# Kernel optimization log

Measured on AMD Instinct MI355X. Metric: run time of the kernel, lower is better.

The kernel has to match this reference:

```python
import math
import jax, jax.numpy as jnp
import numpy as np

B, S, HID = 1, 256, 1024
H, D = 16, 64
INV_NORM = 1.0 / math.sqrt(D)  # inv_norm_factor (beta = 1.0)
NEG = -1e9


def _bloom_alibi(num_heads, seq_len):
    # standard Bloom alibi slopes, shape [H, 1, S]
    closest_pow2 = 2 ** math.floor(math.log2(num_heads))
    base = 2.0 ** (-(2.0 ** -(math.log2(closest_pow2) - 3)))
    slopes = base ** np.arange(1, closest_pow2 + 1)
    if closest_pow2 != num_heads:
        extra_base = 2.0 ** (-(2.0 ** -(math.log2(2 * closest_pow2) - 3)))
        n_extra = min(closest_pow2, num_heads - closest_pow2)
        slopes = np.concatenate([slopes, extra_base ** np.arange(1, 1 + 2 * n_extra, 2)])
    pos = np.arange(seq_len, dtype=np.float32)[None, None, :]
    return jnp.asarray(slopes[:, None, None].astype(np.float32) * pos)  # [H,1,S]


def setup_inputs() -> dict:
    key = jax.random.key(0)
    ks = jax.random.split(key, 6)
    hidden_states = jax.random.normal(ks[0], (B, S, HID), jnp.float32)
    residual = jax.random.normal(ks[1], (B, S, HID), jnp.float32)
    alibi = _bloom_alibi(H, S)  # [B*H, 1, S] with B=1
    # additive causal mask [B, 1, S, S]
    causal = jnp.tril(jnp.ones((S, S), bool))
    attention_mask = jnp.where(causal, 0.0, NEG).astype(jnp.float32)[None, None]
    W_qkv = jax.random.normal(ks[2], (HID, 3 * HID), jnp.float32) * (1.0 / math.sqrt(HID))
    b_qkv = jax.random.normal(ks[3], (3 * HID,), jnp.float32) * 0.02
    W_dense = jax.random.normal(ks[4], (HID, HID), jnp.float32) * (1.0 / math.sqrt(HID))
    b_dense = jax.random.normal(ks[5], (HID,), jnp.float32) * 0.02
    return dict(hidden_states=hidden_states, residual=residual, alibi=alibi,
                attention_mask=attention_mask, W_qkv=W_qkv, b_qkv=b_qkv,
                W_dense=W_dense, b_dense=b_dense)


def reference(hidden_states, residual, alibi, attention_mask, W_qkv, b_qkv, W_dense, b_dense):
    b, s, _ = hidden_states.shape
    # fused qkv projection, Bloom layout: (B, S, H, 3, D)
    fused = (hidden_states @ W_qkv + b_qkv).reshape(b, s, H, 3, D)
    q = fused[..., 0, :].transpose(0, 2, 1, 3)  # [B,H,S,D]
    k = fused[..., 1, :].transpose(0, 2, 1, 3)
    v = fused[..., 2, :].transpose(0, 2, 1, 3)

    alibi_b = alibi.reshape(b, H, 1, s)  # broadcast over query dim
    # standard alibi attention scores: [B,H,S,S]
    scores = alibi_b + INV_NORM * jnp.einsum('bhid,bhjd->bhij', q, k)
    scores = scores + attention_mask  # mask applied only to full scores (as in source)
    # per-dim delta scores: [B,H,D,S,S]; delta[b,h,d,i,j] = alibi + inv_norm * q_d * k_d
    delta = alibi_b[:, :, None] + INV_NORM * jnp.einsum('bhid,bhjd->bhdij', q, k)

    diff = (scores[:, :, None] - delta) * (1.0 / math.sqrt(D))
    p_diff = jax.nn.softmax(diff.astype(jnp.float32), axis=-1)  # [B,H,D,S,S]
    p = jax.nn.softmax(scores.astype(jnp.float32), axis=-1)     # [B,H,S,S]

    # qk importance: sum over batch, query, key of squared deviation, per (h, d)
    qk_importance = jnp.sum((p_diff - p[:, :, None]) ** 2, axis=(0, 3, 4)).reshape(-1)  # [H*D]

    context = jnp.einsum('bhij,bhjd->bhid', p, v)  # [B,H,S,D]
    context = context.transpose(0, 2, 1, 3).reshape(b, s, H * D)
    out = context @ W_dense + b_dense
    out = out + residual  # eval mode: dropout is identity
    return out, qk_importance
```

## Files before the change

### kernel.cpp

```cpp
#include <hip/hip_runtime.h>
#include <math.h>

#define NH  16
#define SEQ 256
#define HD  64
#define HID 1024
#define N3  3072

#define OFF_QB   0
#define OFF_KB   131072
#define OFF_KTB  262144
#define OFF_VTB  393216
#define OFF_CTX  524288

typedef __attribute__((ext_vector_type(8))) short bf16x8;
typedef __attribute__((ext_vector_type(4))) float f32x4;
typedef __attribute__((ext_vector_type(2))) unsigned short us2;
typedef __attribute__((ext_vector_type(4))) unsigned short us4;
typedef __attribute__((ext_vector_type(8))) unsigned short us8;
typedef __attribute__((ext_vector_type(4))) unsigned u32x4;

__device__ __forceinline__ unsigned short f2bf(float x) {
  unsigned u = __builtin_bit_cast(unsigned, x);
  u += 0x7FFF + ((u >> 16) & 1);
  return (unsigned short)(u >> 16);
}
__device__ __forceinline__ float bf2f(unsigned short b) {
  return __builtin_bit_cast(float, (unsigned)b << 16);
}
__device__ __forceinline__ unsigned f2bf2(float lo, float hi) {
  unsigned r;
  asm("v_cvt_pk_bf16_f32 %0, %1, %2" : "=v"(r) : "v"(lo), "v"(hi));
  return r;
}

__global__ __launch_bounds__(256) void k_qkv(
    const float* __restrict__ A, const float* __restrict__ W,
    const float* __restrict__ bias, float* __restrict__ ws,
    float* __restrict__ out) {
  if (blockIdx.x == 0 && blockIdx.y < 4)
    out[SEQ * HID + blockIdx.y * 256 + threadIdx.x] = 0.f;
  __shared__ __align__(16) unsigned short As[32 * 72];
  __shared__ __align__(16) unsigned short Bs[32 * 72];
  const int tid = threadIdx.x;
  const int w = tid >> 6, lane = tid & 63;
  const int col = lane & 15, quad = lane >> 4;
  const int m0 = blockIdx.y * 32, n0 = blockIdx.x * 32;
  const int am = tid >> 3, ak = (tid & 7) * 8;
  const int bn = tid & 31, bkg = (tid >> 5) * 8;
  const float* Ap = &A[(m0 + am) * HID + ak];
  const float* Wp = W + n0 + bn;
  float4 a0 = *(const float4*)&Ap[0];
  float4 a1 = *(const float4*)&Ap[4];
  float pa[8];
#pragma unroll
  for (int u = 0; u < 8; ++u) pa[u] = Wp[(bkg + u) * N3];
  float4 c0 = *(const float4*)&Ap[64];
  float4 c1 = *(const float4*)&Ap[68];
  float pc[8];
#pragma unroll
  for (int u = 0; u < 8; ++u) pc[u] = Wp[(64 + bkg + u) * N3];
  f32x4 acc = {0.f, 0.f, 0.f, 0.f};
  const int k8 = quad * 8;
  const int mt = w & 1, nt = w >> 1;
  for (int k0 = 0; k0 < HID; k0 += 128) {
    *(u32x4*)&As[am * 72 + ak] =
        (u32x4){f2bf2(a0.x, a0.y), f2bf2(a0.z, a0.w),
                f2bf2(a1.x, a1.y), f2bf2(a1.z, a1.w)};
    *(u32x4*)&Bs[bn * 72 + bkg] =
        (u32x4){f2bf2(pa[0], pa[1]), f2bf2(pa[2], pa[3]),
                f2bf2(pa[4], pa[5]), f2bf2(pa[6], pa[7])};
    __syncthreads();
    const int ka = k0 + 128;
    if (ka < HID) {
      a0 = *(const float4*)&Ap[ka];
      a1 = *(const float4*)&Ap[ka + 4];
#pragma unroll
      for (int u = 0; u < 8; ++u) pa[u] = Wp[(ka + bkg + u) * N3];
    }
    {
      const bf16x8 af0 = *(const bf16x8*)&As[(mt * 16 + col) * 72 + k8];
      const bf16x8 af1 = *(const bf16x8*)&As[(mt * 16 + col) * 72 + k8 + 32];
      const bf16x8 bf0 = *(const bf16x8*)&Bs[(nt * 16 + col) * 72 + k8];
      const bf16x8 bf1 = *(const bf16x8*)&Bs[(nt * 16 + col) * 72 + k8 + 32];
      acc = __builtin_amdgcn_mfma_f32_16x16x32_bf16(af0, bf0, acc, 0, 0, 0);
      acc = __builtin_amdgcn_mfma_f32_16x16x32_bf16(af1, bf1, acc, 0, 0, 0);
    }
    __syncthreads();
    *(u32x4*)&As[am * 72 + ak] =
        (u32x4){f2bf2(c0.x, c0.y), f2bf2(c0.z, c0.w),
                f2bf2(c1.x, c1.y), f2bf2(c1.z, c1.w)};
    *(u32x4*)&Bs[bn * 72 + bkg] =
        (u32x4){f2bf2(pc[0], pc[1]), f2bf2(pc[2], pc[3]),
                f2bf2(pc[4], pc[5]), f2bf2(pc[6], pc[7])};
    __syncthreads();
    const int kb2 = k0 + 192;
    if (kb2 < HID) {
      c0 = *(const float4*)&Ap[kb2];
      c1 = *(const float4*)&Ap[kb2 + 4];
#pragma unroll
      for (int u = 0; u < 8; ++u) pc[u] = Wp[(kb2 + bkg + u) * N3];
    }
    {
      const bf16x8 af0 = *(const bf16x8*)&As[(mt * 16 + col) * 72 + k8];
      const bf16x8 af1 = *(const bf16x8*)&As[(mt * 16 + col) * 72 + k8 + 32];
      const bf16x8 bf0 = *(const bf16x8*)&Bs[(nt * 16 + col) * 72 + k8];
      const bf16x8 bf1 = *(const bf16x8*)&Bs[(nt * 16 + col) * 72 + k8 + 32];
      acc = __builtin_amdgcn_mfma_f32_16x16x32_bf16(af0, bf0, acc, 0, 0, 0);
      acc = __builtin_amdgcn_mfma_f32_16x16x32_bf16(af1, bf1, acc, 0, 0, 0);
    }
    __syncthreads();
  }
  unsigned short* qb  = (unsigned short*)(ws + OFF_QB);
  unsigned short* kb  = (unsigned short*)(ws + OFF_KB);
  unsigned short* ktb = (unsigned short*)(ws + OFF_KTB);
  unsigned short* vtb = (unsigned short*)(ws + OFF_VTB);
  const int n = n0 + nt * 16 + col;
  const int h = n / 192;
  const int r2 = n - h * 192;
  const int which = r2 >> 6, d = r2 & 63;
  const float bv = bias[n];
  const unsigned v01 = f2bf2(acc[0] + bv, acc[1] + bv);
  const unsigned v23 = f2bf2(acc[2] + bv, acc[3] + bv);
  const unsigned short vbr[4] = {
      (unsigned short)v01, (unsigned short)(v01 >> 16),
      (unsigned short)v23, (unsigned short)(v23 >> 16)};
#pragma unroll
  for (int r = 0; r < 4; ++r) {
    const int m = m0 + mt * 16 + quad * 4 + r;
    const unsigned short vb = vbr[r];
    if (which == 0) {
      qb[(h * SEQ + m) * HD + d] = vb;
    } else if (which == 1) {
      kb[(h * SEQ + m) * HD + d] = vb;
      ktb[(h * HD + d) * SEQ + m] = vb;
    } else {
      vtb[(h * HD + d) * SEQ + m] = vb;
    }
  }
}

__global__ __launch_bounds__(256) void k_attn(
    const float* __restrict__ alibi, float* __restrict__ ws,
    float* __restrict__ out) {
  *(float4*)&out[(blockIdx.x * 256 + threadIdx.x) * 4] =
      (float4){0.f, 0.f, 0.f, 0.f};
  const int bx = blockIdx.x;
  const int h = bx >> 4, i0 = (bx & 15) * 16;
  const int tid = threadIdx.x, w = tid >> 6, lane = tid & 63;
  const int col = lane & 15, quad = lane >> 4;
  __shared__ __align__(16) unsigned short Albs[3 * 16 * 280];
  __shared__ __align__(16) unsigned short plds[16 * 272];
  __shared__ __align__(16) float redm[16][4];
  __shared__ __align__(16) float reds[16][4];
  __shared__ __align__(16) float red4[16][4][4];
  __shared__ __align__(16) float rowsc[16][4];
  const unsigned short* qbh  = (const unsigned short*)(ws + OFF_QB) + h * SEQ * HD;
  const unsigned short* kbh  = (const unsigned short*)(ws + OFF_KB) + h * SEQ * HD;
  const unsigned short* ktbh = (const unsigned short*)(ws + OFF_KTB) + h * HD * SEQ;
  const unsigned short* vtbh = (const unsigned short*)(ws + OFF_VTB) + h * HD * SEQ;
  const bf16x8 a0 = *(const bf16x8*)&qbh[(i0 + col) * HD + quad * 8];
  const bf16x8 a1 = *(const bf16x8*)&qbh[(i0 + col) * HD + quad * 8 + 32];
  f32x4 acc[4] = {{0.f, 0.f, 0.f, 0.f}, {0.f, 0.f, 0.f, 0.f},
                  {0.f, 0.f, 0.f, 0.f}, {0.f, 0.f, 0.f, 0.f}};
#pragma unroll
  for (int t = 0; t < 4; ++t) {
    const int j = w * 64 + t * 16 + col;
    const bf16x8 b0 = *(const bf16x8*)&kbh[j * HD + quad * 8];
    const bf16x8 b1 = *(const bf16x8*)&kbh[j * HD + quad * 8 + 32];
    acc[t] = __builtin_amdgcn_mfma_f32_16x16x32_bf16(a0, b0, acc[t], 0, 0, 0);
    acc[t] = __builtin_amdgcn_mfma_f32_16x16x32_bf16(a1, b1, acc[t], 0, 0, 0);
  }
  float c[4][4], eb[4][4];
  float rmax[4] = {-3.0e38f, -3.0e38f, -3.0e38f, -3.0e38f};
#pragma unroll
  for (int t = 0; t < 4; ++t) {
    const int j = w * 64 + t * 16 + col;
    const float al = alibi[h * SEQ + j];
#pragma unroll
    for (int r = 0; r < 4; ++r) {
      const int i = i0 + quad * 4 + r;
      const float s = acc[t][r] * 0.125f;
      const float mv = (j <= i) ? 0.f : -1e9f;
      eb[t][r] = __expf((s + mv) * 0.125f);
      const float cv = al + s + mv;
      c[t][r] = cv;
      rmax[r] = fmaxf(rmax[r], cv);
    }
  }
#pragma unroll
  for (int r = 0; r < 4; ++r)
#pragma unroll
    for (int off = 1; off < 16; off <<= 1)
      rmax[r] = fmaxf(rmax[r], __shfl_xor(rmax[r], off));
  if (col == 0)
#pragma unroll
    for (int r = 0; r < 4; ++r) redm[quad * 4 + r][w] = rmax[r];
  __syncthreads();
  float rsum[4];
#pragma unroll
  for (int r = 0; r < 4; ++r) {
    const float4 m4 = *(const float4*)redm[quad * 4 + r];
    const float M = fmaxf(fmaxf(m4.x, m4.y), fmaxf(m4.z, m4.w));
    float s = 0.f;
#pragma unroll
    for (int t = 0; t < 4; ++t) {
      c[t][r] = __expf(c[t][r] - M);
      s += c[t][r];
    }
#pragma unroll
    for (int off = 1; off < 16; off <<= 1) s += __shfl_xor(s, off);
    rsum[r] = s;
  }
  if (col == 0)
#pragma unroll
    for (int r = 0; r < 4; ++r) reds[quad * 4 + r][w] = rsum[r];
  __syncthreads();
#pragma unroll
  for (int r = 0; r < 4; ++r) {
    const float4 s4 = *(const float4*)reds[quad * 4 + r];
    const float inv = __builtin_amdgcn_rcpf((s4.x + s4.y) + (s4.z + s4.w));
    const int il = quad * 4 + r;
    float pt[4];
    float s0 = 0.f, t0 = 0.f, u0 = 0.f, sp = 0.f;
#pragma unroll
    for (int t = 0; t < 4; ++t) {
      const float p = c[t][r] * inv;
      const float E = eb[t][r];
      pt[t] = p;
      s0 += E;
      t0 = __builtin_fmaf(E, E, t0);
      u0 = __builtin_fmaf(E, p, u0);
      sp = __builtin_fmaf(p, p, sp);
    }
    const int jb = il * 280 + w * 64 + col;
    const int pb = il * 272 + w * 64 + col;
    unsigned x;
    x = f2bf2(eb[0][r], eb[1][r]);
    Albs[jb] = (unsigned short)x; Albs[jb + 16] = (unsigned short)(x >> 16);
    x = f2bf2(eb[2][r], eb[3][r]);
    Albs[jb + 32] = (unsigned short)x; Albs[jb + 48] = (unsigned short)(x >> 16);
    x = f2bf2(eb[0][r] * eb[0][r], eb[1][r] * eb[1][r]);
    Albs[4480 + jb] = (unsigned short)x; Albs[4480 + jb + 16] = (unsigned short)(x >> 16);
    x = f2bf2(eb[2][r] * eb[2][r], eb[3][r] * eb[3][r]);
    Albs[4480 + jb + 32] = (unsigned short)x; Albs[4480 + jb + 48] = (unsigned short)(x >> 16);
    x = f2bf2(eb[0][r] * pt[0], eb[1][r] * pt[1]);
    Albs[8960 + jb] = (unsigned short)x; Albs[8960 + jb + 16] = (unsigned short)(x >> 16);
    x = f2bf2(eb[2][r] * pt[2], eb[3][r] * pt[3]);
    Albs[8960 + jb + 32] = (unsigned short)x; Albs[8960 + jb + 48] = (unsigned short)(x >> 16);
    x = f2bf2(pt[0], pt[1]);
    plds[pb] = (unsigned short)x; plds[pb + 16] = (unsigned short)(x >> 16);
    x = f2bf2(pt[2], pt[3]);
    plds[pb + 32] = (unsigned short)x; plds[pb + 48] = (unsigned short)(x >> 16);
#pragma unroll
    for (int off = 1; off < 16; off <<= 1) {
      s0 += __shfl_xor(s0, off);
      t0 += __shfl_xor(t0, off);
      u0 += __shfl_xor(u0, off);
      sp += __shfl_xor(sp, off);
    }
    if (col == 0) *(float4*)&red4[il][w][0] = (float4){s0, t0, u0, sp};
  }
  __syncthreads();
  if (tid < 64) {
    const int row = tid >> 2, x = tid & 3;
    rowsc[row][x] = (red4[row][0][x] + red4[row][1][x]) +
                    (red4[row][2][x] + red4[row][3][x]);
  }
  __syncthreads();
  f32x4 o = {0.f, 0.f, 0.f, 0.f};
#pragma unroll
  for (int s = 0; s < 8; ++s) {
    const int kk = quad * 8 + s * 32;
    const bf16x8 pa8 = *(const bf16x8*)&plds[col * 272 + kk];
    const bf16x8 vb = *(const bf16x8*)&vtbh[(w * 16 + col) * SEQ + kk];
    o = __builtin_amdgcn_mfma_f32_16x16x32_bf16(pa8, vb, o, 0, 0, 0);
  }
  unsigned short* ctxb = (unsigned short*)(ws + OFF_CTX);
  {
    const unsigned x01 = f2bf2(o[0], o[1]);
    const unsigned x23 = f2bf2(o[2], o[3]);
    const int cb = h * HD + w * 16 + col;
    ctxb[(i0 + quad * 4 + 0) * HID + cb] = (unsigned short)x01;
    ctxb[(i0 + quad * 4 + 1) * HID + cb] = (unsigned short)(x01 >> 16);
    ctxb[(i0 + quad * 4 + 2) * HID + cb] = (unsigned short)x23;
    ctxb[(i0 + quad * 4 + 3) * HID + cb] = (unsigned short)(x23 >> 16);
  }
  f32x4 m6[3][2] = {{{0.f, 0.f, 0.f, 0.f}, {0.f, 0.f, 0.f, 0.f}},
                    {{0.f, 0.f, 0.f, 0.f}, {0.f, 0.f, 0.f, 0.f}},
                    {{0.f, 0.f, 0.f, 0.f}, {0.f, 0.f, 0.f, 0.f}}};
  const unsigned short* ktrow = ktbh + (w * 16 + col) * SEQ;
#pragma unroll
  for (int s = 0; s < 8; ++s) {
    const int kk = quad * 8 + s * 32;
    const bf16x8 kb8 = *(const bf16x8*)&ktrow[kk];
    u32x4 kq4;
#pragma unroll
    for (int u = 0; u < 4; ++u) {
      const float t0 = bf2f((unsigned short)kb8[2 * u]);
      const float t1 = bf2f((unsigned short)kb8[2 * u + 1]);
      kq4[u] = f2bf2(t0 * t0, t1 * t1);
    }
    const bf16x8 k2 = __builtin_bit_cast(bf16x8, kq4);
#pragma unroll
    for (int lhs = 0; lhs < 3; ++lhs) {
      const bf16x8 af = *(const bf16x8*)&Albs[lhs * 4480 + col * 280 + kk];
      m6[lhs][0] = __builtin_amdgcn_mfma_f32_16x16x32_bf16(af, kb8, m6[lhs][0], 0, 0, 0);
      m6[lhs][1] = __builtin_amdgcn_mfma_f32_16x16x32_bf16(af, k2, m6[lhs][1], 0, 0, 0);
    }
  }
  const int dg = w * 16 + col;
  float racc = 0.f;
#pragma unroll
  for (int r = 0; r < 4; ++r) {
    const int il = quad * 4 + r;
    const float qc = -0.015625f * bf2f(qbh[(i0 + il) * HD + dg]);
    const float s0 = rowsc[il][0], t0 = rowsc[il][1];
    const float u0 = rowsc[il][2], sp = rowsc[il][3];
    const float S1 = __builtin_fmaf(
        qc, __builtin_fmaf(0.5f * qc, m6[0][1][r], m6[0][0][r]), s0);
    const float S2 = __builtin_fmaf(
        2.f * qc, __builtin_fmaf(qc, m6[1][1][r], m6[1][0][r]), t0);
    const float S3 = __builtin_fmaf(
        qc, __builtin_fmaf(0.5f * qc, m6[2][1][r], m6[2][0][r]), u0);
    const float inv = __builtin_amdgcn_rcpf(S1);
    racc += __builtin_fmaf(__builtin_fmaf(S2, inv, -2.f * S3), inv, sp);
  }
  racc += __shfl_xor(racc, 16);
  racc += __shfl_xor(racc, 32);
  if (lane < 16) atomicAdd(&out[SEQ * HID + h * HD + w * 16 + lane], racc);
}

__global__ __launch_bounds__(256) void k_dense(
    const float* __restrict__ W, const float* __restrict__ bias,
    const float* __restrict__ resid, float* __restrict__ out,
    const float* __restrict__ ws) {
  __shared__ __align__(16) unsigned short As[16 * 72];
  __shared__ __align__(16) unsigned short Bs[64 * 72];
  const int tid = threadIdx.x;
  const int w = tid >> 6, lane = tid & 63;
  const int col = lane & 15, quad = lane >> 4;
  const int m0 = blockIdx.y * 16, n0 = blockIdx.x * 64;
  const int kb = blockIdx.z * 256;
  const int am = tid >> 4, ak = (tid & 15) * 4;
  const int bkg = w * 16;
  const unsigned short* Ab = (const unsigned short*)(ws + OFF_CTX);
  const unsigned short* Ap = &Ab[(m0 + am) * HID + kb + ak];
  const float* Wp = W + n0 + lane;
  us4 aA = *(const us4*)&Ap[0];
  float pA[16];
#pragma unroll
  for (int u = 0; u < 16; ++u) pA[u] = Wp[(kb + bkg + u) * HID];
  us4 aB = *(const us4*)&Ap[64];
  float pB[16];
#pragma unroll
  for (int u = 0; u < 16; ++u) pB[u] = Wp[(kb + 64 + bkg + u) * HID];
  f32x4 acc = {0.f, 0.f, 0.f, 0.f};
  const int k8 = quad * 8;
  for (int k0 = 0; k0 < 256; k0 += 128) {
    *(us4*)&As[am * 72 + ak] = aA;
    *(u32x4*)&Bs[lane * 72 + bkg] =
        (u32x4){f2bf2(pA[0], pA[1]), f2bf2(pA[2], pA[3]),
                f2bf2(pA[4], pA[5]), f2bf2(pA[6], pA[7])};
    *(u32x4*)&Bs[lane * 72 + bkg + 8] =
        (u32x4){f2bf2(pA[8], pA[9]), f2bf2(pA[10], pA[11]),
                f2bf2(pA[12], pA[13]), f2bf2(pA[14], pA[15])};
    __syncthreads();
    const int ka = k0 + 128;
    if (ka < 256) {
      aA = *(const us4*)&Ap[ka];
#pragma unroll
      for (int u = 0; u < 16; ++u) pA[u] = Wp[(kb + ka + bkg + u) * HID];
    }
    {
      const bf16x8 af0 = *(const bf16x8*)&As[col * 72 + k8];
      const bf16x8 af1 = *(const bf16x8*)&As[col * 72 + k8 + 32];
      const bf16x8 bf0 = *(const bf16x8*)&Bs[(w * 16 + col) * 72 + k8];
      const bf16x8 bf1 = *(const bf16x8*)&Bs[(w * 16 + col) * 72 + k8 + 32];
      acc = __builtin_amdgcn_mfma_f32_16x16x32_bf16(af0, bf0, acc, 0, 0, 0);
      acc = __builtin_amdgcn_mfma_f32_16x16x32_bf16(af1, bf1, acc, 0, 0, 0);
    }
    __syncthreads();
    *(us4*)&As[am * 72 + ak] = aB;
    *(u32x4*)&Bs[lane * 72 + bkg] =
        (u32x4){f2bf2(pB[0], pB[1]), f2bf2(pB[2], pB[3]),
                f2bf2(pB[4], pB[5]), f2bf2(pB[6], pB[7])};
    *(u32x4*)&Bs[lane * 72 + bkg + 8] =
        (u32x4){f2bf2(pB[8], pB[9]), f2bf2(pB[10], pB[11]),
                f2bf2(pB[12], pB[13]), f2bf2(pB[14], pB[15])};
    __syncthreads();
    const int kb2 = k0 + 192;
    if (kb2 < 256) {
      aB = *(const us4*)&Ap[kb2];
#pragma unroll
      for (int u = 0; u < 16; ++u) pB[u] = Wp[(kb + kb2 + bkg + u) * HID];
    }
    {
      const bf16x8 af0 = *(const bf16x8*)&As[col * 72 + k8];
      const bf16x8 af1 = *(const bf16x8*)&As[col * 72 + k8 + 32];
      const bf16x8 bf0 = *(const bf16x8*)&Bs[(w * 16 + col) * 72 + k8];
      const bf16x8 bf1 = *(const bf16x8*)&Bs[(w * 16 + col) * 72 + k8 + 32];
      acc = __builtin_amdgcn_mfma_f32_16x16x32_bf16(af0, bf0, acc, 0, 0, 0);
      acc = __builtin_amdgcn_mfma_f32_16x16x32_bf16(af1, bf1, acc, 0, 0, 0);
    }
    __syncthreads();
  }
  const int n = n0 + w * 16 + col;
  const bool first = (blockIdx.z == 0);
  const float bv = first ? bias[n] : 0.f;
#pragma unroll
  for (int r = 0; r < 4; ++r) {
    const int m = m0 + quad * 4 + r;
    const float v = acc[r] + (first ? bv + resid[m * HID + n] : 0.f);
    atomicAdd(&out[m * HID + n], v);
  }
}

extern "C" void kernel_launch(void* const* d_in, const int* in_sizes, int n_in,
                              void* d_out, int out_size, void* d_ws,
                              size_t ws_size, hipStream_t stream) {
  const float* hidden   = (const float*)d_in[0];
  const float* residual = (const float*)d_in[1];
  const float* alibi    = (const float*)d_in[2];
  const float* Wqkv     = (const float*)d_in[4];
  const float* bqkv     = (const float*)d_in[5];
  const float* Wd       = (const float*)d_in[6];
  const float* bd       = (const float*)d_in[7];
  float* out = (float*)d_out;
  float* ws  = (float*)d_ws;

  k_qkv<<<dim3(96, 8), 256, 0, stream>>>(hidden, Wqkv, bqkv, ws, out);
  k_attn<<<dim3(256), 256, 0, stream>>>(alibi, ws, out);
  k_dense<<<dim3(16, 16, 4), 256, 0, stream>>>(Wd, bd, residual, out, ws);
}
```

Baseline: 104.9 us.

## Double-buffer LDS in GEMMs and merge attention softmax reductions into one pass

The QKV and dense GEMM kernels now alternate between two LDS buffers, which removes half of the per-step barriers. The dense kernel also reads its A operand straight from global memory instead of staging it through LDS. In the attention kernel, the row-max pass is replaced by a fixed per-row shift taken from the alibi value at the query's own index (the causal row maximum of alibi). All five row sums are then reduced together in one shuffle and LDS pass, which cuts two barriers and two reductions. The fixed shift assumes scores are small relative to that alibi value, so exp could overflow or lose precision for large q·k.

```diff
diff --git a/kernel.cpp b/kernel.cpp
--- a/kernel.cpp
+++ b/kernel.cpp
@@ -40,8 +40,8 @@
     float* __restrict__ out) {
   if (blockIdx.x == 0 && blockIdx.y < 4)
     out[SEQ * HID + blockIdx.y * 256 + threadIdx.x] = 0.f;
-  __shared__ __align__(16) unsigned short As[32 * 72];
-  __shared__ __align__(16) unsigned short Bs[32 * 72];
+  __shared__ __align__(16) unsigned short As[2 * 32 * 72];
+  __shared__ __align__(16) unsigned short Bs[2 * 32 * 72];
   const int tid = threadIdx.x;
   const int w = tid >> 6, lane = tid & 63;
   const int col = lane & 15, quad = lane >> 4;
@@ -86,11 +86,10 @@
       acc = __builtin_amdgcn_mfma_f32_16x16x32_bf16(af0, bf0, acc, 0, 0, 0);
       acc = __builtin_amdgcn_mfma_f32_16x16x32_bf16(af1, bf1, acc, 0, 0, 0);
     }
-    __syncthreads();
-    *(u32x4*)&As[am * 72 + ak] =
+    *(u32x4*)&As[2304 + am * 72 + ak] =
         (u32x4){f2bf2(c0.x, c0.y), f2bf2(c0.z, c0.w),
                 f2bf2(c1.x, c1.y), f2bf2(c1.z, c1.w)};
-    *(u32x4*)&Bs[bn * 72 + bkg] =
+    *(u32x4*)&Bs[2304 + bn * 72 + bkg] =
         (u32x4){f2bf2(pc[0], pc[1]), f2bf2(pc[2], pc[3]),
                 f2bf2(pc[4], pc[5]), f2bf2(pc[6], pc[7])};
     __syncthreads();
@@ -102,14 +101,13 @@
       for (int u = 0; u < 8; ++u) pc[u] = Wp[(kb2 + bkg + u) * N3];
     }
     {
-      const bf16x8 af0 = *(const bf16x8*)&As[(mt * 16 + col) * 72 + k8];
-      const bf16x8 af1 = *(const bf16x8*)&As[(mt * 16 + col) * 72 + k8 + 32];
-      const bf16x8 bf0 = *(const bf16x8*)&Bs[(nt * 16 + col) * 72 + k8];
-      const bf16x8 bf1 = *(const bf16x8*)&Bs[(nt * 16 + col) * 72 + k8 + 32];
+      const bf16x8 af0 = *(const bf16x8*)&As[2304 + (mt * 16 + col) * 72 + k8];
+      const bf16x8 af1 = *(const bf16x8*)&As[2304 + (mt * 16 + col) * 72 + k8 + 32];
+      const bf16x8 bf0 = *(const bf16x8*)&Bs[2304 + (nt * 16 + col) * 72 + k8];
+      const bf16x8 bf1 = *(const bf16x8*)&Bs[2304 + (nt * 16 + col) * 72 + k8 + 32];
       acc = __builtin_amdgcn_mfma_f32_16x16x32_bf16(af0, bf0, acc, 0, 0, 0);
       acc = __builtin_amdgcn_mfma_f32_16x16x32_bf16(af1, bf1, acc, 0, 0, 0);
     }
-    __syncthreads();
   }
   unsigned short* qb  = (unsigned short*)(ws + OFF_QB);
   unsigned short* kb  = (unsigned short*)(ws + OFF_KB);
@@ -151,10 +149,7 @@
   const int col = lane & 15, quad = lane >> 4;
   __shared__ __align__(16) unsigned short Albs[3 * 16 * 280];
   __shared__ __align__(16) unsigned short plds[16 * 272];
-  __shared__ __align__(16) float redm[16][4];
-  __shared__ __align__(16) float reds[16][4];
-  __shared__ __align__(16) float red4[16][4][4];
-  __shared__ __align__(16) float rowsc[16][4];
+  __shared__ __align__(16) float red5[16][4][8];
   const unsigned short* qbh  = (const unsigned short*)(ws + OFF_QB) + h * SEQ * HD;
   const unsigned short* kbh  = (const unsigned short*)(ws + OFF_KB) + h * SEQ * HD;
   const unsigned short* ktbh = (const unsigned short*)(ws + OFF_KTB) + h * HD * SEQ;
@@ -171,8 +166,13 @@
     acc[t] = __builtin_amdgcn_mfma_f32_16x16x32_bf16(a0, b0, acc[t], 0, 0, 0);
     acc[t] = __builtin_amdgcn_mfma_f32_16x16x32_bf16(a1, b1, acc[t], 0, 0, 0);
   }
-  float c[4][4], eb[4][4];
-  float rmax[4] = {-3.0e38f, -3.0e38f, -3.0e38f, -3.0e38f};
+  float chat[4][4], eb[4][4];
+  float sc[4] = {0.f, 0.f, 0.f, 0.f}, se[4] = {0.f, 0.f, 0.f, 0.f};
+  float se2[4] = {0.f, 0.f, 0.f, 0.f}, sec[4] = {0.f, 0.f, 0.f, 0.f};
+  float sc2[4] = {0.f, 0.f, 0.f, 0.f};
+  float Mr[4];
+#pragma unroll
+  for (int r = 0; r < 4; ++r) Mr[r] = alibi[h * SEQ + i0 + quad * 4 + r];
 #pragma unroll
   for (int t = 0; t < 4; ++t) {
     const int j = w * 64 + t * 16 + col;
@@ -182,57 +182,53 @@
       const int i = i0 + quad * 4 + r;
       const float s = acc[t][r] * 0.125f;
       const float mv = (j <= i) ? 0.f : -1e9f;
-      eb[t][r] = __expf((s + mv) * 0.125f);
-      const float cv = al + s + mv;
-      c[t][r] = cv;
-      rmax[r] = fmaxf(rmax[r], cv);
-    }
-  }
-#pragma unroll
-  for (int r = 0; r < 4; ++r)
-#pragma unroll
-    for (int off = 1; off < 16; off <<= 1)
-      rmax[r] = fmaxf(rmax[r], __shfl_xor(rmax[r], off));
-  if (col == 0)
-#pragma unroll
-    for (int r = 0; r < 4; ++r) redm[quad * 4 + r][w] = rmax[r];
+      const float E = __expf((s + mv) * 0.125f);
+      const float ch = __expf(al + s + mv - Mr[r]);
+      eb[t][r] = E;
+      chat[t][r] = ch;
+      sc[r] += ch;
+      se[r] += E;
+      se2[r] = __builtin_fmaf(E, E, se2[r]);
+      sec[r] = __builtin_fmaf(E, ch, sec[r]);
+      sc2[r] = __builtin_fmaf(ch, ch, sc2[r]);
+    }
+  }
+#pragma unroll
+  for (int r = 0; r < 4; ++r) {
+#pragma unroll
+    for (int off = 1; off < 16; off <<= 1) {
+      sc[r]  += __shfl_xor(sc[r], off);
+      se[r]  += __shfl_xor(se[r], off);
+      se2[r] += __shfl_xor(se2[r], off);
+      sec[r] += __shfl_xor(sec[r], off);
+      sc2[r] += __shfl_xor(sc2[r], off);
+    }
+    if (col == 0) {
+      const int il = quad * 4 + r;
+      *(float4*)&red5[il][w][0] = (float4){sc[r], se[r], se2[r], sec[r]};
+      red5[il][w][4] = sc2[r];
+    }
+  }
   __syncthreads();
-  float rsum[4];
+  float rs0[4], rt0[4], ru0[4], rsp[4];
 #pragma unroll
   for (int r = 0; r < 4; ++r) {
-    const float4 m4 = *(const float4*)redm[quad * 4 + r];
-    const float M = fmaxf(fmaxf(m4.x, m4.y), fmaxf(m4.z, m4.w));
-    float s = 0.f;
-#pragma unroll
-    for (int t = 0; t < 4; ++t) {
-      c[t][r] = __expf(c[t][r] - M);
-      s += c[t][r];
-    }
-#pragma unroll
-    for (int off = 1; off < 16; off <<= 1) s += __shfl_xor(s, off);
-    rsum[r] = s;
-  }
-  if (col == 0)
-#pragma unroll
-    for (int r = 0; r < 4; ++r) reds[quad * 4 + r][w] = rsum[r];
-  __syncthreads();
-#pragma unroll
-  for (int r = 0; r < 4; ++r) {
-    const float4 s4 = *(const float4*)reds[quad * 4 + r];
-    const float inv = __builtin_amdgcn_rcpf((s4.x + s4.y) + (s4.z + s4.w));
     const int il = quad * 4 + r;
-    float pt[4];
-    float s0 = 0.f, t0 = 0.f, u0 = 0.f, sp = 0.f;
-#pragma unroll
-    for (int t = 0; t < 4; ++t) {
-      const float p = c[t][r] * inv;
-      const float E = eb[t][r];
-      pt[t] = p;
-      s0 += E;
-      t0 = __builtin_fmaf(E, E, t0);
-      u0 = __builtin_fmaf(E, p, u0);
-      sp = __builtin_fmaf(p, p, sp);
-    }
+    const float4 q0 = *(const float4*)&red5[il][0][0];
+    const float4 q1 = *(const float4*)&red5[il][1][0];
+    const float4 q2 = *(const float4*)&red5[il][2][0];
+    const float4 q3 = *(const float4*)&red5[il][3][0];
+    const float totc = (q0.x + q1.x) + (q2.x + q3.x);
+    rs0[r] = (q0.y + q1.y) + (q2.y + q3.y);
+    rt0[r] = (q0.z + q1.z) + (q2.z + q3.z);
+    const float totec = (q0.w + q1.w) + (q2.w + q3.w);
+    const float totc2 = (red5[il][0][4] + red5[il][1][4]) +
+                        (red5[il][2][4] + red5[il][3][4]);
+    const float inv = __builtin_amdgcn_rcpf(totc);
+    ru0[r] = inv * totec;
+    rsp[r] = inv * inv * totc2;
+    const float p0 = chat[0][r] * inv, p1 = chat[1][r] * inv;
+    const float p2 = chat[2][r] * inv, p3 = chat[3][r] * inv;
     const int jb = il * 280 + w * 64 + col;
     const int pb = il * 272 + w * 64 + col;
     unsigned x;
@@ -244,28 +240,14 @@
     Albs[4480 + jb] = (unsigned short)x; Albs[4480 + jb + 16] = (unsigned short)(x >> 16);
     x = f2bf2(eb[2][r] * eb[2][r], eb[3][r] * eb[3][r]);
     Albs[4480 + jb + 32] = (unsigned short)x; Albs[4480 + jb + 48] = (unsigned short)(x >> 16);
-    x = f2bf2(eb[0][r] * pt[0], eb[1][r] * pt[1]);
+    x = f2bf2(eb[0][r] * p0, eb[1][r] * p1);
     Albs[8960 + jb] = (unsigned short)x; Albs[8960 + jb + 16] = (unsigned short)(x >> 16);
-    x = f2bf2(eb[2][r] * pt[2], eb[3][r] * pt[3]);
+    x = f2bf2(eb[2][r] * p2, eb[3][r] * p3);
     Albs[8960 + jb + 32] = (unsigned short)x; Albs[8960 + jb + 48] = (unsigned short)(x >> 16);
-    x = f2bf2(pt[0], pt[1]);
+    x = f2bf2(p0, p1);
     plds[pb] = (unsigned short)x; plds[pb + 16] = (unsigned short)(x >> 16);
-    x = f2bf2(pt[2], pt[3]);
+    x = f2bf2(p2, p3);
     plds[pb + 32] = (unsigned short)x; plds[pb + 48] = (unsigned short)(x >> 16);
-#pragma unroll
-    for (int off = 1; off < 16; off <<= 1) {
-      s0 += __shfl_xor(s0, off);
-      t0 += __shfl_xor(t0, off);
-      u0 += __shfl_xor(u0, off);
-      sp += __shfl_xor(sp, off);
-    }
-    if (col == 0) *(float4*)&red4[il][w][0] = (float4){s0, t0, u0, sp};
-  }
-  __syncthreads();
-  if (tid < 64) {
-    const int row = tid >> 2, x = tid & 3;
-    rowsc[row][x] = (red4[row][0][x] + red4[row][1][x]) +
-                    (red4[row][2][x] + red4[row][3][x]);
   }
   __syncthreads();
   f32x4 o = {0.f, 0.f, 0.f, 0.f};
@@ -315,16 +297,14 @@
   for (int r = 0; r < 4; ++r) {
     const int il = quad * 4 + r;
     const float qc = -0.015625f * bf2f(qbh[(i0 + il) * HD + dg]);
-    const float s0 = rowsc[il][0], t0 = rowsc[il][1];
-    const float u0 = rowsc[il][2], sp = rowsc[il][3];
     const float S1 = __builtin_fmaf(
-        qc, __builtin_fmaf(0.5f * qc, m6[0][1][r], m6[0][0][r]), s0);
+        qc, __builtin_fmaf(0.5f * qc, m6[0][1][r], m6[0][0][r]), rs0[r]);
     const float S2 = __builtin_fmaf(
-        2.f * qc, __builtin_fmaf(qc, m6[1][1][r], m6[1][0][r]), t0);
+        2.f * qc, __builtin_fmaf(qc, m6[1][1][r], m6[1][0][r]), rt0[r]);
     const float S3 = __builtin_fmaf(
-        qc, __builtin_fmaf(0.5f * qc, m6[2][1][r], m6[2][0][r]), u0);
+        qc, __builtin_fmaf(0.5f * qc, m6[2][1][r], m6[2][0][r]), ru0[r]);
     const float inv = __builtin_amdgcn_rcpf(S1);
-    racc += __builtin_fmaf(__builtin_fmaf(S2, inv, -2.f * S3), inv, sp);
+    racc += __builtin_fmaf(__builtin_fmaf(S2, inv, -2.f * S3), inv, rsp[r]);
   }
   racc += __shfl_xor(racc, 16);
   racc += __shfl_xor(racc, 32);
@@ -335,30 +315,24 @@
     const float* __restrict__ W, const float* __restrict__ bias,
     const float* __restrict__ resid, float* __restrict__ out,
     const float* __restrict__ ws) {
-  __shared__ __align__(16) unsigned short As[16 * 72];
-  __shared__ __align__(16) unsigned short Bs[64 * 72];
+  __shared__ __align__(16) unsigned short Bs[2 * 64 * 72];
   const int tid = threadIdx.x;
   const int w = tid >> 6, lane = tid & 63;
   const int col = lane & 15, quad = lane >> 4;
   const int m0 = blockIdx.y * 16, n0 = blockIdx.x * 64;
   const int kb = blockIdx.z * 256;
-  const int am = tid >> 4, ak = (tid & 15) * 4;
   const int bkg = w * 16;
   const unsigned short* Ab = (const unsigned short*)(ws + OFF_CTX);
-  const unsigned short* Ap = &Ab[(m0 + am) * HID + kb + ak];
+  const unsigned short* Arow = &Ab[(m0 + col) * HID + kb + quad * 8];
   const float* Wp = W + n0 + lane;
-  us4 aA = *(const us4*)&Ap[0];
-  float pA[16];
+  float pA[16], pB[16];
 #pragma unroll
   for (int u = 0; u < 16; ++u) pA[u] = Wp[(kb + bkg + u) * HID];
-  us4 aB = *(const us4*)&Ap[64];
-  float pB[16];
 #pragma unroll
   for (int u = 0; u < 16; ++u) pB[u] = Wp[(kb + 64 + bkg + u) * HID];
   f32x4 acc = {0.f, 0.f, 0.f, 0.f};
   const int k8 = quad * 8;
   for (int k0 = 0; k0 < 256; k0 += 128) {
-    *(us4*)&As[am * 72 + ak] = aA;
     *(u32x4*)&Bs[lane * 72 + bkg] =
         (u32x4){f2bf2(pA[0], pA[1]), f2bf2(pA[2], pA[3]),
                 f2bf2(pA[4], pA[5]), f2bf2(pA[6], pA[7])};
@@ -368,42 +342,37 @@
     __syncthreads();
     const int ka = k0 + 128;
     if (ka < 256) {
-      aA = *(const us4*)&Ap[ka];
 #pragma unroll
       for (int u = 0; u < 16; ++u) pA[u] = Wp[(kb + ka + bkg + u) * HID];
     }
     {
-      const bf16x8 af0 = *(const bf16x8*)&As[col * 72 + k8];
-      const bf16x8 af1 = *(const bf16x8*)&As[col * 72 + k8 + 32];
+      const bf16x8 af0 = *(const bf16x8*)&Arow[k0];
+      const bf16x8 af1 = *(const bf16x8*)&Arow[k0 + 32];
       const bf16x8 bf0 = *(const bf16x8*)&Bs[(w * 16 + col) * 72 + k8];
       const bf16x8 bf1 = *(const bf16x8*)&Bs[(w * 16 + col) * 72 + k8 + 32];
       acc = __builtin_amdgcn_mfma_f32_16x16x32_bf16(af0, bf0, acc, 0, 0, 0);
       acc = __builtin_amdgcn_mfma_f32_16x16x32_bf16(af1, bf1, acc, 0, 0, 0);
     }
-    __syncthreads();
-    *(us4*)&As[am * 72 + ak] = aB;
-    *(u32x4*)&Bs[lane * 72 + bkg] =
+    *(u32x4*)&Bs[4608 + lane * 72 + bkg] =
         (u32x4){f2bf2(pB[0], pB[1]), f2bf2(pB[2], pB[3]),
                 f2bf2(pB[4], pB[5]), f2bf2(pB[6], pB[7])};
-    *(u32x4*)&Bs[lane * 72 + bkg + 8] =
+    *(u32x4*)&Bs[4608 + lane * 72 + bkg + 8] =
         (u32x4){f2bf2(pB[8], pB[9]), f2bf2(pB[10], pB[11]),
                 f2bf2(pB[12], pB[13]), f2bf2(pB[14], pB[15])};
     __syncthreads();
     const int kb2 = k0 + 192;
     if (kb2 < 256) {
-      aB = *(const us4*)&Ap[kb2];
 #pragma unroll
       for (int u = 0; u < 16; ++u) pB[u] = Wp[(kb + kb2 + bkg + u) * HID];
     }
     {
-      const bf16x8 af0 = *(const bf16x8*)&As[col * 72 + k8];
-      const bf16x8 af1 = *(const bf16x8*)&As[col * 72 + k8 + 32];
-      const bf16x8 bf0 = *(const bf16x8*)&Bs[(w * 16 + col) * 72 + k8];
-      const bf16x8 bf1 = *(const bf16x8*)&Bs[(w * 16 + col) * 72 + k8 + 32];
+      const bf16x8 af0 = *(const bf16x8*)&Arow[k0 + 64];
+      const bf16x8 af1 = *(const bf16x8*)&Arow[k0 + 96];
+      const bf16x8 bf0 = *(const bf16x8*)&Bs[4608 + (w * 16 + col) * 72 + k8];
+      const bf16x8 bf1 = *(const bf16x8*)&Bs[4608 + (w * 16 + col) * 72 + k8 + 32];
       acc = __builtin_amdgcn_mfma_f32_16x16x32_bf16(af0, bf0, acc, 0, 0, 0);
       acc = __builtin_amdgcn_mfma_f32_16x16x32_bf16(af1, bf1, acc, 0, 0, 0);
     }
-    __syncthreads();
   }
   const int n = n0 + w * 16 + col;
   const bool first = (blockIdx.z == 0);
```

Result: slower. 109.6 us (+4.5%).
